# Kernel tuning notes

Hardware: AMD Instinct MI355X
Metric: run time of the kernel (lower is better)

## Reference

```python
import jax, jax.numpy as jnp
import numpy as np

D_MODEL = 1024
N_HEADS = 16
HEAD_DIM = D_MODEL // N_HEADS
L = 2048


def setup_inputs() -> dict:
    key = jax.random.key(0)
    ks = jax.random.split(key, 7)
    x = jax.random.normal(ks[0], (L, D_MODEL), dtype=jnp.float32)
    pair_bias = jax.random.normal(ks[1], (N_HEADS, L, L), dtype=jnp.float32)
    gate = jax.random.uniform(ks[2], (N_HEADS, 1, 1), dtype=jnp.float32)
    # Learned params (Linear stores weight [out, in]; y = x @ W.T + b)
    s_qkv = 1.0 / np.sqrt(D_MODEL)
    W_qkv = jax.random.uniform(ks[3], (3 * D_MODEL, D_MODEL), minval=-s_qkv, maxval=s_qkv, dtype=jnp.float32)
    b_qkv = jax.random.uniform(ks[4], (3 * D_MODEL,), minval=-s_qkv, maxval=s_qkv, dtype=jnp.float32)
    W_out = jax.random.uniform(ks[5], (D_MODEL, D_MODEL), minval=-s_qkv, maxval=s_qkv, dtype=jnp.float32)
    b_out = jax.random.uniform(ks[6], (D_MODEL,), minval=-s_qkv, maxval=s_qkv, dtype=jnp.float32)
    return {"x": x, "pair_bias": pair_bias, "gate": gate,
            "W_qkv": W_qkv, "b_qkv": b_qkv, "W_out": W_out, "b_out": b_out}


def reference(x, pair_bias, gate, W_qkv, b_qkv, W_out, b_out):
    Lx = x.shape[0]
    scale = HEAD_DIM ** -0.5
    qkv = (x @ W_qkv.T + b_qkv).reshape(Lx, 3, N_HEADS, HEAD_DIM)
    q, k, v = qkv[:, 0], qkv[:, 1], qkv[:, 2]  # [L, H, Dh]
    logits = jnp.einsum('ihd,jhd->hij', q, k) * scale + gate * pair_bias
    attn = jax.nn.softmax(logits, axis=-1)  # dropout p=0 (eval) -> identity
    out = jnp.einsum('hij,jhd->ihd', attn, v).reshape(Lx, D_MODEL)
    return out @ W_out.T + b_out
```

## Files before the change

### kernel.cpp

```cpp
#include <hip/hip_runtime.h>
#include <cstdint>
#include <cstddef>

#define L_SEQ  2048
#define DMODEL 1024
#define NHEADS 16
#define HDIM   64
#define NQKV   3072
#define JC     512

typedef float f32x4 __attribute__((ext_vector_type(4)));
typedef short s16x8 __attribute__((ext_vector_type(8)));

static __device__ __forceinline__ unsigned short f2bf(float f) {
  unsigned u = __float_as_uint(f);
  return (unsigned short)((u + 0x7fffu + ((u >> 16) & 1u)) >> 16);
}

static __device__ __forceinline__ float bf2f(unsigned short u) {
  return __uint_as_float(((unsigned)u) << 16);
}

static __device__ __forceinline__ void gld_lds16(void* lds, const void* g) {
  __builtin_amdgcn_global_load_lds(
      (const __attribute__((address_space(1))) void*)g,
      (__attribute__((address_space(3))) void*)lds, 16, 0, 0);
}

__global__ __launch_bounds__(256) void cvt_kernel(
    const float* __restrict__ x, const float* __restrict__ wqkv,
    const float* __restrict__ wout,
    unsigned short* __restrict__ xb, unsigned short* __restrict__ wqkvb,
    unsigned short* __restrict__ woutb) {
  const int NX = L_SEQ * DMODEL / 4;
  const int NW1 = NQKV * DMODEL / 4;
  const int NW2 = DMODEL * DMODEL / 4;
  const int tot = NX + NW1 + NW2;
  for (int i = blockIdx.x * blockDim.x + threadIdx.x; i < tot;
       i += gridDim.x * blockDim.x) {
    const float4* s;
    unsigned short* d;
    int j;
    if (i < NX) { s = (const float4*)x; d = xb; j = i; }
    else if (i < NX + NW1) { s = (const float4*)wqkv; d = wqkvb; j = i - NX; }
    else { s = (const float4*)wout; d = woutb; j = i - NX - NW1; }
    float4 v = s[j];
    ushort4 o;
    o.x = f2bf(v.x); o.y = f2bf(v.y); o.z = f2bf(v.z); o.w = f2bf(v.w);
    *(ushort4*)(d + 4 * (size_t)j) = o;
  }
}

template <int KDIM>
static __device__ __forceinline__ void gemm_bt_core(
    const unsigned short* __restrict__ A, const unsigned short* __restrict__ Bt,
    unsigned short* As, unsigned short* Bs, int bm, int bn, f32x4 acc[4][4]) {
  const int tid = threadIdx.x;
  const int lane = tid & 63;
  const int wave = tid >> 6;
  const int g = lane >> 4;
  const int li = lane & 15;
  const int wm = (wave >> 1) * 64;
  const int wn = (wave & 1) * 64;
  const int arow = tid >> 2;
  const int acolb = (tid & 3) << 4;
  const char* gA = (const char*)A + (size_t)(bm * 128 + arow) * (KDIM * 2) + acolb;
  const char* gB = (const char*)Bt + (size_t)(bn * 128 + arow) * (KDIM * 2) + acolb;
  char* lA = (char*)As + wave * 1024;
  char* lB = (char*)Bs + wave * 1024;
  const size_t half = (size_t)64 * KDIM * 2;
  for (int kt = 0; kt < KDIM; kt += 32) {
    __syncthreads();
    gld_lds16(lA, gA + kt * 2);
    gld_lds16(lA + 4096, gA + half + kt * 2);
    gld_lds16(lB, gB + kt * 2);
    gld_lds16(lB + 4096, gB + half + kt * 2);
    __syncthreads();
    const s16x8* Av = (const s16x8*)As;
    const s16x8* Bv = (const s16x8*)Bs;
    s16x8 af[4], bfv[4];
#pragma unroll
    for (int mt = 0; mt < 4; ++mt) af[mt] = Av[(wm + mt * 16 + li) * 4 + g];
#pragma unroll
    for (int nt = 0; nt < 4; ++nt) bfv[nt] = Bv[(wn + nt * 16 + li) * 4 + g];
#pragma unroll
    for (int mt = 0; mt < 4; ++mt)
#pragma unroll
      for (int nt = 0; nt < 4; ++nt)
        acc[mt][nt] = __builtin_amdgcn_mfma_f32_16x16x32_bf16(
            af[mt], bfv[nt], acc[mt][nt], 0, 0, 0);
  }
}

__global__ __launch_bounds__(256, 2) void gemm_qkv_k(
    const unsigned short* __restrict__ A, const unsigned short* __restrict__ Bt,
    const float* __restrict__ bqkv, unsigned short* __restrict__ Qb,
    unsigned short* __restrict__ Kb, unsigned short* __restrict__ Vt) {
  __shared__ alignas(16) unsigned short As[128 * 32], Bs[128 * 32];
  f32x4 acc[4][4] = {};
  gemm_bt_core<DMODEL>(A, Bt, As, Bs, blockIdx.x, blockIdx.y, acc);
  const int lane = threadIdx.x & 63, wave = threadIdx.x >> 6;
  const int g = lane >> 4, li = lane & 15;
  const int wm = (wave >> 1) * 64, wn = (wave & 1) * 64;
#pragma unroll
  for (int mt = 0; mt < 4; ++mt)
#pragma unroll
    for (int nt = 0; nt < 4; ++nt)
#pragma unroll
      for (int r = 0; r < 4; ++r) {
        int i = blockIdx.x * 128 + wm + mt * 16 + 4 * g + r;
        int n = blockIdx.y * 128 + wn + nt * 16 + li;
        float v = acc[mt][nt][r] + bqkv[n];
        int s = n >> 10;
        int h = (n >> 6) & 15;
        int d = n & 63;
        if (s == 0)      Qb[(((size_t)h * L_SEQ + i) << 6) + d] = f2bf(v * 0.125f);
        else if (s == 1) Kb[(((size_t)h * L_SEQ + i) << 6) + d] = f2bf(v);
        else             Vt[(size_t)(h * 64 + d) * L_SEQ + i] = f2bf(v);
      }
}

__global__ __launch_bounds__(256) void attn_score_k(
    const unsigned short* __restrict__ Qb, const unsigned short* __restrict__ Kb,
    const float* __restrict__ bias, const float* __restrict__ gate,
    unsigned short* __restrict__ E) {
  __shared__ alignas(16) float blds[16][JC];
  __shared__ alignas(16) char plds[4 * 2048];
  const int h = blockIdx.z, it = blockIdx.x, jc = blockIdx.y;
  const int i0 = it * 16;
  const int tid = threadIdx.x, lane = tid & 63, wave = tid >> 6;
  const int g = lane >> 4, li = lane & 15;
  char* myP = plds + wave * 2048;
  const float* bh = bias + (size_t)h * L_SEQ * L_SEQ + (size_t)i0 * L_SEQ + jc * JC;
#pragma unroll
  for (int q = 0; q < 4; ++q) {
    const int r = 4 * wave + q;
    const char* gsrc = (const char*)(bh + (size_t)r * L_SEQ) + lane * 16;
    gld_lds16(&blds[r][0], gsrc);
    gld_lds16(&blds[r][256], gsrc + 1024);
  }
  const s16x8* Qv = (const s16x8*)(Qb + (((size_t)h * L_SEQ + i0) << 6));
  const s16x8 qf0 = Qv[li * 8 + g];
  const s16x8 qf1 = Qv[li * 8 + 4 + g];
  const float gh = gate[h];
  const s16x8* Kall = (const s16x8*)(Kb + (((size_t)h * L_SEQ) << 6));
  __syncthreads();
#pragma unroll
  for (int st = 0; st < 2; ++st) {
    const int c0 = wave * 128 + st * 64;
    const int jg = jc * JC + c0;
    s16x8 k0[4], k1[4];
#pragma unroll
    for (int nt = 0; nt < 4; ++nt) {
      k0[nt] = Kall[(jg + nt * 16 + li) * 8 + g];
      k1[nt] = Kall[(jg + nt * 16 + li) * 8 + 4 + g];
    }
    f32x4 s[4];
#pragma unroll
    for (int nt = 0; nt < 4; ++nt) {
      f32x4 z = {0.f, 0.f, 0.f, 0.f};
      z = __builtin_amdgcn_mfma_f32_16x16x32_bf16(qf0, k0[nt], z, 0, 0, 0);
      z = __builtin_amdgcn_mfma_f32_16x16x32_bf16(qf1, k1[nt], z, 0, 0, 0);
      s[nt] = z;
    }
#pragma unroll
    for (int nt = 0; nt < 4; ++nt)
#pragma unroll
      for (int r = 0; r < 4; ++r) {
        const int row = 4 * g + r;
        float p = __expf(fmaf(gh, blds[row][c0 + nt * 16 + li], s[nt][r]));
        unsigned b = (unsigned)(row * 128 + (nt * 16 + li) * 2) ^
                     (unsigned)((row & 7) << 4);
        *(unsigned short*)(myP + b) = f2bf(p);
      }
    asm volatile("s_waitcnt lgkmcnt(0)" ::: "memory");
    const unsigned b0 = ((unsigned)(li * 128 + 16 * g)) ^ (unsigned)((li & 7) << 4);
    const unsigned b1 = ((unsigned)(li * 128 + 64 + 16 * g)) ^ (unsigned)((li & 7) << 4);
    const s16x8 pa0 = *(const s16x8*)(myP + b0);
    const s16x8 pa1 = *(const s16x8*)(myP + b1);
    const int js = jc * 8 + wave * 2 + st;
    unsigned short* Eo =
        E + ((((size_t)h * 128 + it) * 32 + js) * 128 + lane) * 8;
    *(s16x8*)Eo = pa0;
    *(s16x8*)(Eo + 512) = pa1;
  }
}

__global__ __launch_bounds__(256) void attn_pv_k(
    const unsigned short* __restrict__ E, const unsigned short* __restrict__ Vt,
    unsigned short* __restrict__ AO) {
  __shared__ alignas(16) char lds[16 * 1024 + 256];
  const int h = blockIdx.y, it = blockIdx.x;
  const int i0 = it * 16;
  const int tid = threadIdx.x, lane = tid & 63, wave = tid >> 6;
  const int g = lane >> 4, li = lane & 15;
  const size_t ebase = ((size_t)h * 128 + it) * 32 * 128;
  f32x4 accO[4] = {};
  float lsum = 0.f;
#pragma unroll
  for (int t = 0; t < 8; ++t) {
    const int js = t * 4 + wave;
    const int j0 = js * 64;
    const unsigned short* Eo = E + (ebase + (size_t)js * 128 + lane) * 8;
    const s16x8 pa0 = *(const s16x8*)Eo;
    const s16x8 pa1 = *(const s16x8*)(Eo + 512);
#pragma unroll
    for (int e = 0; e < 8; ++e)
      lsum += bf2f((unsigned short)pa0[e]) + bf2f((unsigned short)pa1[e]);
#pragma unroll
    for (int dt = 0; dt < 4; ++dt) {
      const unsigned short* vb = Vt + (size_t)(h * 64 + dt * 16 + li) * L_SEQ + j0;
      const s16x8 v0 = *(const s16x8*)(vb + 8 * g);
      const s16x8 v1 = *(const s16x8*)(vb + 32 + 8 * g);
      accO[dt] = __builtin_amdgcn_mfma_f32_16x16x32_bf16(pa0, v0, accO[dt], 0, 0, 0);
      accO[dt] = __builtin_amdgcn_mfma_f32_16x16x32_bf16(pa1, v1, accO[dt], 0, 0, 0);
    }
  }
  lsum += __shfl_xor(lsum, 16);
  lsum += __shfl_xor(lsum, 32);
  float* accL = (float*)lds;
  float* lL = (float*)(lds + 16 * 1024);
#pragma unroll
  for (int dt = 0; dt < 4; ++dt)
#pragma unroll
    for (int r = 0; r < 4; ++r)
      accL[(wave * 16 + 4 * g + r) * 64 + dt * 16 + li] = accO[dt][r];
  if (lane < 16) lL[wave * 16 + lane] = lsum;
  __syncthreads();
  {
    const int row = tid >> 4;
    const int c0 = (tid & 15) * 4;
    f32x4 sum = {0.f, 0.f, 0.f, 0.f};
    float ls = 0.f;
#pragma unroll
    for (int w = 0; w < 4; ++w) {
      const f32x4 a = *(const f32x4*)&accL[(w * 16 + row) * 64 + c0];
      sum += a;
      ls += lL[w * 16 + row];
    }
    const float inv = 1.0f / ls;
    ushort4 o;
    o.x = f2bf(sum[0] * inv);
    o.y = f2bf(sum[1] * inv);
    o.z = f2bf(sum[2] * inv);
    o.w = f2bf(sum[3] * inv);
    *(ushort4*)(AO + (size_t)(i0 + row) * DMODEL + h * 64 + c0) = o;
  }
}

__global__ __launch_bounds__(256, 2) void gemm_out_k(
    const unsigned short* __restrict__ A, const unsigned short* __restrict__ Bt,
    const float* __restrict__ bout, float* __restrict__ out) {
  __shared__ alignas(16) unsigned short As[128 * 32], Bs[128 * 32];
  f32x4 acc[4][4] = {};
  gemm_bt_core<DMODEL>(A, Bt, As, Bs, blockIdx.x, blockIdx.y, acc);
  const int lane = threadIdx.x & 63, wave = threadIdx.x >> 6;
  const int g = lane >> 4, li = lane & 15;
  const int wm = (wave >> 1) * 64, wn = (wave & 1) * 64;
#pragma unroll
  for (int mt = 0; mt < 4; ++mt)
#pragma unroll
    for (int nt = 0; nt < 4; ++nt)
#pragma unroll
      for (int r = 0; r < 4; ++r) {
        int i = blockIdx.x * 128 + wm + mt * 16 + 4 * g + r;
        int n = blockIdx.y * 128 + wn + nt * 16 + li;
        out[(size_t)i * DMODEL + n] = acc[mt][nt][r] + bout[n];
      }
}

extern "C" void kernel_launch(void* const* d_in, const int* in_sizes, int n_in,
                              void* d_out, int out_size, void* d_ws,
                              size_t ws_size, hipStream_t stream) {
  const float* x = (const float*)d_in[0];
  const float* pb = (const float*)d_in[1];
  const float* gate = (const float*)d_in[2];
  const float* wqkv = (const float*)d_in[3];
  const float* bqkv = (const float*)d_in[4];
  const float* wout = (const float*)d_in[5];
  const float* bout = (const float*)d_in[6];

  unsigned short* ws = (unsigned short*)d_ws;
  unsigned short* xb = ws;
  unsigned short* wqkvb = xb + (size_t)L_SEQ * DMODEL;
  unsigned short* woutb = wqkvb + (size_t)NQKV * DMODEL;
  unsigned short* Qb = woutb + (size_t)DMODEL * DMODEL;
  unsigned short* Kb = Qb + (size_t)NHEADS * L_SEQ * HDIM;
  unsigned short* Vt = Kb + (size_t)NHEADS * L_SEQ * HDIM;
  unsigned short* AO = Vt + (size_t)NHEADS * L_SEQ * HDIM;
  unsigned short* E  = AO + (size_t)L_SEQ * DMODEL;

  cvt_kernel<<<1024, 256, 0, stream>>>(x, wqkv, wout, xb, wqkvb, woutb);
  gemm_qkv_k<<<dim3(16, 24), 256, 0, stream>>>(xb, wqkvb, bqkv, Qb, Kb, Vt);
  attn_score_k<<<dim3(128, 4, 16), 256, 0, stream>>>(Qb, Kb, pb, gate, E);
  attn_pv_k<<<dim3(128, 16), 256, 0, stream>>>(E, Vt, AO);
  gemm_out_k<<<dim3(16, 8), 256, 0, stream>>>(AO, woutb, bout, (float*)d_out);
}
```

Baseline: 236.3 us.

## Fuse PV product into score kernel with split-J partial outputs and combine

The score kernel now multiplies the bf16 probabilities directly by V and accumulates row sums in registers, writing fp32 partial outputs and denominators per J-chunk. A small combine kernel sums the four chunks and normalizes. This removes the round trip of the full bf16 exp-score matrix E through global memory, at the cost of fp32 partial buffers and an extra launch. As before, softmax is computed without max subtraction.

```diff
diff --git a/kernel.cpp b/kernel.cpp
--- a/kernel.cpp
+++ b/kernel.cpp
@@ -120,18 +120,21 @@
       }
 }
 
-__global__ __launch_bounds__(256) void attn_score_k(
+__global__ __launch_bounds__(256) void attn_fused_k(
     const unsigned short* __restrict__ Qb, const unsigned short* __restrict__ Kb,
-    const float* __restrict__ bias, const float* __restrict__ gate,
-    unsigned short* __restrict__ E) {
+    const unsigned short* __restrict__ Vt, const float* __restrict__ bias,
+    const float* __restrict__ gate, float* __restrict__ partO,
+    float* __restrict__ partD) {
   __shared__ alignas(16) float blds[16][JC];
   __shared__ alignas(16) char plds[4 * 2048];
+  __shared__ float dls[4][16];
   const int h = blockIdx.z, it = blockIdx.x, jc = blockIdx.y;
   const int i0 = it * 16;
   const int tid = threadIdx.x, lane = tid & 63, wave = tid >> 6;
   const int g = lane >> 4, li = lane & 15;
   char* myP = plds + wave * 2048;
-  const float* bh = bias + (size_t)h * L_SEQ * L_SEQ + (size_t)i0 * L_SEQ + jc * JC;
+  const float* bh =
+      bias + (size_t)h * L_SEQ * L_SEQ + (size_t)i0 * L_SEQ + jc * JC;
 #pragma unroll
   for (int q = 0; q < 4; ++q) {
     const int r = 4 * wave + q;
@@ -144,6 +147,8 @@
   const s16x8 qf1 = Qv[li * 8 + 4 + g];
   const float gh = gate[h];
   const s16x8* Kall = (const s16x8*)(Kb + (((size_t)h * L_SEQ) << 6));
+  f32x4 accO[4] = {};
+  f32x4 lpart = {0.f, 0.f, 0.f, 0.f};
   __syncthreads();
 #pragma unroll
   for (int st = 0; st < 2; ++st) {
@@ -169,83 +174,84 @@
       for (int r = 0; r < 4; ++r) {
         const int row = 4 * g + r;
         float p = __expf(fmaf(gh, blds[row][c0 + nt * 16 + li], s[nt][r]));
+        unsigned short pb = f2bf(p);
+        lpart[r] += bf2f(pb);
         unsigned b = (unsigned)(row * 128 + (nt * 16 + li) * 2) ^
                      (unsigned)((row & 7) << 4);
-        *(unsigned short*)(myP + b) = f2bf(p);
+        *(unsigned short*)(myP + b) = pb;
       }
     asm volatile("s_waitcnt lgkmcnt(0)" ::: "memory");
     const unsigned b0 = ((unsigned)(li * 128 + 16 * g)) ^ (unsigned)((li & 7) << 4);
     const unsigned b1 = ((unsigned)(li * 128 + 64 + 16 * g)) ^ (unsigned)((li & 7) << 4);
     const s16x8 pa0 = *(const s16x8*)(myP + b0);
     const s16x8 pa1 = *(const s16x8*)(myP + b1);
-    const int js = jc * 8 + wave * 2 + st;
-    unsigned short* Eo =
-        E + ((((size_t)h * 128 + it) * 32 + js) * 128 + lane) * 8;
-    *(s16x8*)Eo = pa0;
-    *(s16x8*)(Eo + 512) = pa1;
-  }
-}
-
-__global__ __launch_bounds__(256) void attn_pv_k(
-    const unsigned short* __restrict__ E, const unsigned short* __restrict__ Vt,
-    unsigned short* __restrict__ AO) {
-  __shared__ alignas(16) char lds[16 * 1024 + 256];
-  const int h = blockIdx.y, it = blockIdx.x;
-  const int i0 = it * 16;
-  const int tid = threadIdx.x, lane = tid & 63, wave = tid >> 6;
-  const int g = lane >> 4, li = lane & 15;
-  const size_t ebase = ((size_t)h * 128 + it) * 32 * 128;
-  f32x4 accO[4] = {};
-  float lsum = 0.f;
-#pragma unroll
-  for (int t = 0; t < 8; ++t) {
-    const int js = t * 4 + wave;
-    const int j0 = js * 64;
-    const unsigned short* Eo = E + (ebase + (size_t)js * 128 + lane) * 8;
-    const s16x8 pa0 = *(const s16x8*)Eo;
-    const s16x8 pa1 = *(const s16x8*)(Eo + 512);
-#pragma unroll
-    for (int e = 0; e < 8; ++e)
-      lsum += bf2f((unsigned short)pa0[e]) + bf2f((unsigned short)pa1[e]);
 #pragma unroll
     for (int dt = 0; dt < 4; ++dt) {
-      const unsigned short* vb = Vt + (size_t)(h * 64 + dt * 16 + li) * L_SEQ + j0;
+      const unsigned short* vb = Vt + (size_t)(h * 64 + dt * 16 + li) * L_SEQ + jg;
       const s16x8 v0 = *(const s16x8*)(vb + 8 * g);
       const s16x8 v1 = *(const s16x8*)(vb + 32 + 8 * g);
       accO[dt] = __builtin_amdgcn_mfma_f32_16x16x32_bf16(pa0, v0, accO[dt], 0, 0, 0);
       accO[dt] = __builtin_amdgcn_mfma_f32_16x16x32_bf16(pa1, v1, accO[dt], 0, 0, 0);
     }
   }
-  lsum += __shfl_xor(lsum, 16);
-  lsum += __shfl_xor(lsum, 32);
-  float* accL = (float*)lds;
-  float* lL = (float*)(lds + 16 * 1024);
+  float lrow[4];
+#pragma unroll
+  for (int r = 0; r < 4; ++r) {
+    float tl = lpart[r];
+    tl += __shfl_xor(tl, 1);
+    tl += __shfl_xor(tl, 2);
+    tl += __shfl_xor(tl, 4);
+    tl += __shfl_xor(tl, 8);
+    lrow[r] = tl;
+  }
+  __syncthreads();
+  float* accL = &blds[0][0];
 #pragma unroll
   for (int dt = 0; dt < 4; ++dt)
 #pragma unroll
     for (int r = 0; r < 4; ++r)
       accL[(wave * 16 + 4 * g + r) * 64 + dt * 16 + li] = accO[dt][r];
-  if (lane < 16) lL[wave * 16 + lane] = lsum;
+  if (li == 0) {
+#pragma unroll
+    for (int r = 0; r < 4; ++r) dls[wave][4 * g + r] = lrow[r];
+  }
   __syncthreads();
   {
     const int row = tid >> 4;
-    const int c0 = (tid & 15) * 4;
+    const int c4 = (tid & 15) * 4;
     f32x4 sum = {0.f, 0.f, 0.f, 0.f};
-    float ls = 0.f;
+    float ds = 0.f;
 #pragma unroll
     for (int w = 0; w < 4; ++w) {
-      const f32x4 a = *(const f32x4*)&accL[(w * 16 + row) * 64 + c0];
-      sum += a;
-      ls += lL[w * 16 + row];
+      sum += *(const f32x4*)&accL[(w * 16 + row) * 64 + c4];
+      ds += dls[w][row];
     }
-    const float inv = 1.0f / ls;
-    ushort4 o;
-    o.x = f2bf(sum[0] * inv);
-    o.y = f2bf(sum[1] * inv);
-    o.z = f2bf(sum[2] * inv);
-    o.w = f2bf(sum[3] * inv);
-    *(ushort4*)(AO + (size_t)(i0 + row) * DMODEL + h * 64 + c0) = o;
-  }
+    const size_t pb = ((size_t)h * 128 + it) * 4 + jc;
+    *(f32x4*)&partO[(pb * 16 + row) * 64 + c4] = sum;
+    if ((tid & 15) == 0) partD[pb * 16 + row] = ds;
+  }
+}
+
+__global__ __launch_bounds__(256) void attn_comb_k(
+    const float* __restrict__ partO, const float* __restrict__ partD,
+    unsigned short* __restrict__ AO) {
+  const int it = blockIdx.x, h = blockIdx.y;
+  const int tid = threadIdx.x, row = tid >> 4, c4 = (tid & 15) * 4;
+  const size_t pb = ((size_t)h * 128 + it) * 4;
+  f32x4 sum = {0.f, 0.f, 0.f, 0.f};
+  float ds = 0.f;
+#pragma unroll
+  for (int c = 0; c < 4; ++c) {
+    sum += *(const f32x4*)&partO[((pb + c) * 16 + row) * 64 + c4];
+    ds += partD[(pb + c) * 16 + row];
+  }
+  const float inv = 1.0f / ds;
+  ushort4 o;
+  o.x = f2bf(sum[0] * inv);
+  o.y = f2bf(sum[1] * inv);
+  o.z = f2bf(sum[2] * inv);
+  o.w = f2bf(sum[3] * inv);
+  *(ushort4*)(AO + (size_t)(it * 16 + row) * DMODEL + h * 64 + c4) = o;
 }
 
 __global__ __launch_bounds__(256, 2) void gemm_out_k(
@@ -288,11 +294,13 @@
   unsigned short* Kb = Qb + (size_t)NHEADS * L_SEQ * HDIM;
   unsigned short* Vt = Kb + (size_t)NHEADS * L_SEQ * HDIM;
   unsigned short* AO = Vt + (size_t)NHEADS * L_SEQ * HDIM;
-  unsigned short* E  = AO + (size_t)L_SEQ * DMODEL;
+  float* partO = (float*)(AO + (size_t)L_SEQ * DMODEL);
+  float* partD = partO + (size_t)8192 * 1024;
 
   cvt_kernel<<<1024, 256, 0, stream>>>(x, wqkv, wout, xb, wqkvb, woutb);
   gemm_qkv_k<<<dim3(16, 24), 256, 0, stream>>>(xb, wqkvb, bqkv, Qb, Kb, Vt);
-  attn_score_k<<<dim3(128, 4, 16), 256, 0, stream>>>(Qb, Kb, pb, gate, E);
-  attn_pv_k<<<dim3(128, 16), 256, 0, stream>>>(E, Vt, AO);
+  attn_fused_k<<<dim3(128, 4, 16), 256, 0, stream>>>(Qb, Kb, Vt, pb, gate,
+                                                     partO, partD);
+  attn_comb_k<<<dim3(128, 16), 256, 0, stream>>>(partO, partD, AO);
   gemm_out_k<<<dim3(16, 8), 256, 0, stream>>>(AO, woutb, bout, (float*)d_out);
 }
```

Measured after the change: 210.8 us. 1.12x faster.
